# Performance work log

Measured on AMD Instinct MI355X. Metric: run time of the kernel, lower is better.

The kernel has to match this reference:

```python
import jax, jax.numpy as jnp
import numpy as np

B, C_IN, C_OUT, MODES, LENGTH = 32, 32, 32, 64, 16384


def dht(x):
    # Discrete Hartley Transform via complex FFT: H = Re(X) - Im(X) = sum x * cas
    X = jnp.fft.fft(x, axis=-1)
    return X.real - X.imag


def flip_periodic(x):
    # Z[0] = x[0], Z[k] = x[N-k] for k >= 1
    return jnp.concatenate([x[..., :1], x[..., 1:][..., ::-1]], axis=-1)


def setup_inputs() -> dict:
    key = jax.random.key(0)
    k1, k2, k3 = jax.random.split(key, 3)
    x = jax.random.normal(k1, (B, C_IN, LENGTH), dtype=jnp.float32)
    scale = 1.0 / (C_IN * C_OUT)
    weights1 = scale * jax.random.uniform(k2, (C_IN, C_OUT, MODES), dtype=jnp.float32)
    phase_weights = jax.random.uniform(k3, (C_IN, C_OUT, MODES), dtype=jnp.float32)
    return {"x": x, "weights1": weights1, "phase_weights": phase_weights}


def reference(x, weights1, phase_weights):
    batch, length = x.shape[0], x.shape[-1]
    m = weights1.shape[-1]
    out_ch = weights1.shape[1]

    x_ht = dht(x)                      # [b, in, L]
    xm = x_ht[:, :, :m]                # truncated spectrum [b, in, m]

    # Hartley convolution theorem: even/odd decomposition of the kernel
    y_flip = flip_periodic(weights1)
    y_even = 0.5 * (weights1 + y_flip)
    y_odd = 0.5 * (weights1 - y_flip)
    z = (jnp.einsum('bix,iox->box', xm, y_even)
         + jnp.einsum('bix,iox->box', flip_periodic(xm), y_odd))  # [b, out, m]

    # phase multiply (per-(out, mode); see notes on original in-place broadcast)
    z = z * jnp.sin(phase_weights)[0]  # [out, m] broadcast over batch

    out_ht = jnp.zeros((batch, out_ch, length), dtype=x.dtype).at[:, :, :m].set(z)
    # inverse DHT: DHT is involutory up to 1/n
    return dht(out_ht) / length
```

## Files before the change

kernel.cpp:

```cpp
#include <hip/hip_runtime.h>
#include <math.h>

#define N_LEN 16384
#define NMODES 64
#define NROWS 1024
#define TWO_PI_OVER_N 3.8349519697141029e-04f
#define PAD 72

typedef __bf16  bf16x8  __attribute__((ext_vector_type(8)));
typedef float   floatx16 __attribute__((ext_vector_type(16)));

__device__ inline unsigned short f2b(float f) {
    unsigned u = __float_as_uint(f);
    u += 0x7fffu + ((u >> 16) & 1u);
    return (unsigned short)(u >> 16);
}

__global__ __launch_bounds__(256) void build_tabs(unsigned short* __restrict__ Ttb,
                                                  unsigned short* __restrict__ Ttn) {
    int idx = blockIdx.x * 256 + threadIdx.x;
    int m, n;
    if (idx < N_LEN * NMODES) { m = idx >> 14; n = idx & (N_LEN - 1); }
    else { int j = idx - N_LEN * NMODES; n = j >> 6; m = j & 63; }
    float s, c;
    sincosf((float)((n * m) & (N_LEN - 1)) * TWO_PI_OVER_N, &s, &c);
    unsigned short v = f2b(c + s);
    if (idx < N_LEN * NMODES) Ttb[idx] = v;
    else                      Ttn[idx - N_LEN * NMODES] = v;
}

#define G1_RB 128

__global__ __launch_bounds__(256) void gemm1(const float* __restrict__ x,
                                             const unsigned short* __restrict__ Ttb,
                                             float* __restrict__ part,
                                             int ntiles) {
    __shared__ unsigned short xs[G1_RB * PAD];
    __shared__ unsigned short ts[64 * PAD];
    const int tid  = threadIdx.x;
    const int lane = tid & 63;
    const int w    = tid >> 6;
    const int q    = lane >> 5;
    const int m    = lane & 31;
    const int row0 = blockIdx.x * G1_RB;
    const int n0   = blockIdx.y * (ntiles * 64);

    floatx16 acc0, acc1;
#pragma unroll
    for (int i = 0; i < 16; ++i) { acc0[i] = 0.f; acc1[i] = 0.f; }

    float4 xr[8];
    uint4  tr[2];
    {
        const int base = n0;
#pragma unroll
        for (int it = 0; it < 8; ++it) {
            int cid = it * 256 + tid, rr = cid >> 4, cc = (cid & 15) * 4;
            xr[it] = *(const float4*)(x + (size_t)(row0 + rr) * N_LEN + base + cc);
        }
#pragma unroll
        for (int it = 0; it < 2; ++it) {
            int idx = it * 256 + tid, mm = idx >> 3, c = idx & 7;
            tr[it] = *(const uint4*)(Ttb + (size_t)mm * N_LEN + base + c * 8);
        }
    }

    for (int t = 0; t < ntiles; ++t) {
        __syncthreads();
#pragma unroll
        for (int it = 0; it < 8; ++it) {
            int cid = it * 256 + tid, rr = cid >> 4, cc = (cid & 15) * 4;
            ushort4 v;
            v.x = f2b(xr[it].x); v.y = f2b(xr[it].y);
            v.z = f2b(xr[it].z); v.w = f2b(xr[it].w);
            *(ushort4*)(xs + rr * PAD + cc) = v;
        }
#pragma unroll
        for (int it = 0; it < 2; ++it) {
            int idx = it * 256 + tid, mm = idx >> 3, c = idx & 7;
            *(uint4*)(ts + mm * PAD + c * 8) = tr[it];
        }
        if (t + 1 < ntiles) {
            const int base = n0 + (t + 1) * 64;
#pragma unroll
            for (int it = 0; it < 8; ++it) {
                int cid = it * 256 + tid, rr = cid >> 4, cc = (cid & 15) * 4;
                xr[it] = *(const float4*)(x + (size_t)(row0 + rr) * N_LEN + base + cc);
            }
#pragma unroll
            for (int it = 0; it < 2; ++it) {
                int idx = it * 256 + tid, mm = idx >> 3, c = idx & 7;
                tr[it] = *(const uint4*)(Ttb + (size_t)mm * N_LEN + base + c * 8);
            }
        }
        __syncthreads();
#pragma unroll
        for (int ks = 0; ks < 4; ++ks) {
            bf16x8 a  = *(const bf16x8*)(xs + (w * 32 + m) * PAD + ks * 16 + q * 8);
            bf16x8 b0 = *(const bf16x8*)(ts + (m)          * PAD + ks * 16 + q * 8);
            bf16x8 b1 = *(const bf16x8*)(ts + (32 + m)     * PAD + ks * 16 + q * 8);
            acc0 = __builtin_amdgcn_mfma_f32_32x32x16_bf16(a, b0, acc0, 0, 0, 0);
            acc1 = __builtin_amdgcn_mfma_f32_32x32x16_bf16(a, b1, acc1, 0, 0, 0);
        }
    }

    float* pb = part + ((size_t)blockIdx.y * NROWS + row0 + w * 32) * NMODES;
#pragma unroll
    for (int r = 0; r < 16; ++r) {
        int rowt = (r & 3) + 8 * (r >> 2) + 4 * q;
        pb[rowt * NMODES + m]      = acc0[r];
        pb[rowt * NMODES + 32 + m] = acc1[r];
    }
}

__global__ __launch_bounds__(256) void reduce_xm(const float* __restrict__ part,
                                                 float* __restrict__ xm, int S) {
    int gid = blockIdx.x * 256 + threadIdx.x;
    float4 a = make_float4(0.f, 0.f, 0.f, 0.f);
#pragma unroll 4
    for (int s = 0; s < S; ++s) {
        float4 v = *(const float4*)(part + (size_t)s * (NROWS * NMODES) + (size_t)gid * 4);
        a.x += v.x; a.y += v.y; a.z += v.z; a.w += v.w;
    }
    *(float4*)(xm + (size_t)gid * 4) = a;
}

__global__ __launch_bounds__(256) void mixk(const float* __restrict__ xm,
                                            const float* __restrict__ w1,
                                            const float* __restrict__ pw,
                                            unsigned short* __restrict__ zb) {
    int k = threadIdx.x & 63;
    int wave = threadIdx.x >> 6;
    int b = blockIdx.x;
    int o = blockIdx.y * 4 + wave;
    int kf = (NMODES - k) & 63;

    float acc = 0.f;
#pragma unroll 4
    for (int i = 0; i < 32; ++i) {
        float xv  = xm[(size_t)(b * 32 + i) * NMODES + k];
        float xvf = xm[(size_t)(b * 32 + i) * NMODES + kf];
        float w   = w1[(size_t)(i * 32 + o) * NMODES + k];
        float wf  = w1[(size_t)(i * 32 + o) * NMODES + kf];
        acc = fmaf(xv, 0.5f * (w + wf), acc);
        acc = fmaf(xvf, 0.5f * (w - wf), acc);
    }
    const float sc = 1.0f / (float)N_LEN;
    zb[(size_t)(b * 32 + o) * NMODES + k] =
        f2b(acc * sinf(pw[(size_t)o * NMODES + k]) * sc);
}

#define G2_NB 256

__global__ __launch_bounds__(256) void gemm2(const unsigned short* __restrict__ Ttn,
                                             const unsigned short* __restrict__ zb,
                                             float* __restrict__ out) {
    __shared__ unsigned short tts[G2_NB * PAD];
    __shared__ unsigned short zs[64 * PAD];
    const int tid  = threadIdx.x;
    const int lane = tid & 63;
    const int w    = tid >> 6;
    const int q    = lane >> 5;
    const int m    = lane & 31;
    const int wr   = w & 1;
    const int wn   = w >> 1;
    const int row0 = blockIdx.x * 64;
    const int nb0  = blockIdx.y * G2_NB;

#pragma unroll
    for (int it = 0; it < 8; ++it) {
        int idx = it * 256 + tid, rr = idx >> 3, c = idx & 7;
        *(uint4*)(tts + rr * PAD + c * 8) =
            *(const uint4*)(Ttn + (size_t)(nb0 + rr) * NMODES + c * 8);
    }
#pragma unroll
    for (int it = 0; it < 2; ++it) {
        int idx = it * 256 + tid, rr = idx >> 3, c = idx & 7;
        *(uint4*)(zs + rr * PAD + c * 8) =
            *(const uint4*)(zb + (size_t)(row0 + rr) * NMODES + c * 8);
    }
    __syncthreads();

    floatx16 acc[4];
#pragma unroll
    for (int nt = 0; nt < 4; ++nt)
#pragma unroll
        for (int i = 0; i < 16; ++i) acc[nt][i] = 0.f;

#pragma unroll
    for (int ks = 0; ks < 4; ++ks) {
        bf16x8 a = *(const bf16x8*)(zs + (wr * 32 + m) * PAD + ks * 16 + q * 8);
#pragma unroll
        for (int nt = 0; nt < 4; ++nt) {
            bf16x8 b = *(const bf16x8*)(tts + (wn * 128 + nt * 32 + m) * PAD + ks * 16 + q * 8);
            acc[nt] = __builtin_amdgcn_mfma_f32_32x32x16_bf16(a, b, acc[nt], 0, 0, 0);
        }
    }

#pragma unroll
    for (int nt = 0; nt < 4; ++nt) {
#pragma unroll
        for (int r = 0; r < 16; ++r) {
            int rowt = (r & 3) + 8 * (r >> 2) + 4 * q;
            out[(size_t)(row0 + wr * 32 + rowt) * N_LEN + nb0 + wn * 128 + nt * 32 + m]
                = acc[nt][r];
        }
    }
}

extern "C" void kernel_launch(void* const* d_in, const int* in_sizes, int n_in,
                              void* d_out, int out_size, void* d_ws, size_t ws_size,
                              hipStream_t stream) {
    const float* x  = (const float*)d_in[0];
    const float* w1 = (const float*)d_in[1];
    const float* pw = (const float*)d_in[2];
    float* out = (float*)d_out;

    int S = 64;
    while (S > 8) {
        size_t need = 2u * (size_t)N_LEN * NMODES * 2u
                    + (size_t)S * NROWS * NMODES * 4u
                    + (size_t)NROWS * NMODES * 4u
                    + (size_t)NROWS * NMODES * 2u;
        if (need <= ws_size) break;
        S >>= 1;
    }
    const int ntiles = N_LEN / S / 64;

    char* p = (char*)d_ws;
    unsigned short* Ttb = (unsigned short*)p;           p += (size_t)N_LEN * NMODES * 2;
    unsigned short* Ttn = (unsigned short*)p;           p += (size_t)N_LEN * NMODES * 2;
    float*          P   = (float*)p;                    p += (size_t)S * NROWS * NMODES * 4;
    float*          XM  = (float*)p;                    p += (size_t)NROWS * NMODES * 4;
    unsigned short* ZB  = (unsigned short*)p;

    build_tabs<<<dim3((2 * N_LEN * NMODES) / 256), dim3(256), 0, stream>>>(Ttb, Ttn);

    gemm1<<<dim3(NROWS / G1_RB, S), dim3(256), 0, stream>>>(x, Ttb, P, ntiles);

    reduce_xm<<<dim3(64), dim3(256), 0, stream>>>(P, XM, S);

    mixk<<<dim3(32, 8), dim3(256), 0, stream>>>(XM, w1, pw, ZB);

    gemm2<<<dim3(NROWS / 64, N_LEN / G2_NB), dim3(256), 0, stream>>>(Ttn, ZB, out);
}
```

Before: 146.4 us.

## Compute cas twiddles inline in both GEMMs instead of building global tables

Removes the build_tabs kernel and the two global bf16 cas tables. gemm1 and gemm2 now compute the cas values on the fly using hardware sin/cos in revolutions and write them straight into shared memory. This drops one launch and the table traffic through global memory, at the cost of redundant transcendental work in every block. reduce_xm is also reshaped to use scalar loads over four times as many threads with four independent accumulators, for more parallelism.

```diff
diff --git a/kernel.cpp b/kernel.cpp
--- a/kernel.cpp
+++ b/kernel.cpp
@@ -4,8 +4,8 @@
 #define N_LEN 16384
 #define NMODES 64
 #define NROWS 1024
-#define TWO_PI_OVER_N 3.8349519697141029e-04f
 #define PAD 72
+#define REV_SCALE 6.103515625e-05f
 
 typedef __bf16  bf16x8  __attribute__((ext_vector_type(8)));
 typedef float   floatx16 __attribute__((ext_vector_type(16)));
@@ -16,23 +16,21 @@
     return (unsigned short)(u >> 16);
 }
 
-__global__ __launch_bounds__(256) void build_tabs(unsigned short* __restrict__ Ttb,
-                                                  unsigned short* __restrict__ Ttn) {
-    int idx = blockIdx.x * 256 + threadIdx.x;
-    int m, n;
-    if (idx < N_LEN * NMODES) { m = idx >> 14; n = idx & (N_LEN - 1); }
-    else { int j = idx - N_LEN * NMODES; n = j >> 6; m = j & 63; }
+__device__ inline unsigned short cas_bf16(unsigned k) {
+    float rev = (float)k * REV_SCALE;
+#if __has_builtin(__builtin_amdgcn_sinf) && __has_builtin(__builtin_amdgcn_cosf)
+    float s = __builtin_amdgcn_sinf(rev);
+    float c = __builtin_amdgcn_cosf(rev);
+#else
     float s, c;
-    sincosf((float)((n * m) & (N_LEN - 1)) * TWO_PI_OVER_N, &s, &c);
-    unsigned short v = f2b(c + s);
-    if (idx < N_LEN * NMODES) Ttb[idx] = v;
-    else                      Ttn[idx - N_LEN * NMODES] = v;
+    sincosf(rev * 6.28318530717958647692f, &s, &c);
+#endif
+    return f2b(c + s);
 }
 
 #define G1_RB 128
 
 __global__ __launch_bounds__(256) void gemm1(const float* __restrict__ x,
-                                             const unsigned short* __restrict__ Ttb,
                                              float* __restrict__ part,
                                              int ntiles) {
     __shared__ unsigned short xs[G1_RB * PAD];
@@ -45,23 +43,20 @@
     const int row0 = blockIdx.x * G1_RB;
     const int n0   = blockIdx.y * (ntiles * 64);
 
+    const int mrow = tid >> 2;
+    const int nl0  = (tid & 3) * 16;
+
     floatx16 acc0, acc1;
 #pragma unroll
     for (int i = 0; i < 16; ++i) { acc0[i] = 0.f; acc1[i] = 0.f; }
 
     float4 xr[8];
-    uint4  tr[2];
     {
         const int base = n0;
 #pragma unroll
         for (int it = 0; it < 8; ++it) {
             int cid = it * 256 + tid, rr = cid >> 4, cc = (cid & 15) * 4;
             xr[it] = *(const float4*)(x + (size_t)(row0 + rr) * N_LEN + base + cc);
-        }
-#pragma unroll
-        for (int it = 0; it < 2; ++it) {
-            int idx = it * 256 + tid, mm = idx >> 3, c = idx & 7;
-            tr[it] = *(const uint4*)(Ttb + (size_t)mm * N_LEN + base + c * 8);
         }
     }
 
@@ -75,11 +70,6 @@
             v.z = f2b(xr[it].z); v.w = f2b(xr[it].w);
             *(ushort4*)(xs + rr * PAD + cc) = v;
         }
-#pragma unroll
-        for (int it = 0; it < 2; ++it) {
-            int idx = it * 256 + tid, mm = idx >> 3, c = idx & 7;
-            *(uint4*)(ts + mm * PAD + c * 8) = tr[it];
-        }
         if (t + 1 < ntiles) {
             const int base = n0 + (t + 1) * 64;
 #pragma unroll
@@ -87,11 +77,20 @@
                 int cid = it * 256 + tid, rr = cid >> 4, cc = (cid & 15) * 4;
                 xr[it] = *(const float4*)(x + (size_t)(row0 + rr) * N_LEN + base + cc);
             }
-#pragma unroll
-            for (int it = 0; it < 2; ++it) {
-                int idx = it * 256 + tid, mm = idx >> 3, c = idx & 7;
-                tr[it] = *(const uint4*)(Ttb + (size_t)mm * N_LEN + base + c * 8);
+        }
+        {
+            unsigned nb = (unsigned)(n0 + t * 64 + nl0);
+            unsigned k  = ((unsigned)mrow * nb) & (N_LEN - 1);
+            unsigned pk[8];
+#pragma unroll
+            for (int j = 0; j < 8; ++j) {
+                unsigned lo = cas_bf16(k); k = (k + mrow) & (N_LEN - 1);
+                unsigned hi = cas_bf16(k); k = (k + mrow) & (N_LEN - 1);
+                pk[j] = lo | (hi << 16);
             }
+            uint4* dst = (uint4*)(ts + mrow * PAD + nl0);
+            dst[0] = make_uint4(pk[0], pk[1], pk[2], pk[3]);
+            dst[1] = make_uint4(pk[4], pk[5], pk[6], pk[7]);
         }
         __syncthreads();
 #pragma unroll
@@ -116,13 +115,16 @@
 __global__ __launch_bounds__(256) void reduce_xm(const float* __restrict__ part,
                                                  float* __restrict__ xm, int S) {
     int gid = blockIdx.x * 256 + threadIdx.x;
-    float4 a = make_float4(0.f, 0.f, 0.f, 0.f);
+    const float* p = part + gid;
+    float a0 = 0.f, a1 = 0.f, a2 = 0.f, a3 = 0.f;
 #pragma unroll 4
-    for (int s = 0; s < S; ++s) {
-        float4 v = *(const float4*)(part + (size_t)s * (NROWS * NMODES) + (size_t)gid * 4);
-        a.x += v.x; a.y += v.y; a.z += v.z; a.w += v.w;
-    }
-    *(float4*)(xm + (size_t)gid * 4) = a;
+    for (int s = 0; s < S; s += 4) {
+        a0 += p[(size_t)(s + 0) * (NROWS * NMODES)];
+        a1 += p[(size_t)(s + 1) * (NROWS * NMODES)];
+        a2 += p[(size_t)(s + 2) * (NROWS * NMODES)];
+        a3 += p[(size_t)(s + 3) * (NROWS * NMODES)];
+    }
+    xm[gid] = (a0 + a1) + (a2 + a3);
 }
 
 __global__ __launch_bounds__(256) void mixk(const float* __restrict__ xm,
@@ -152,8 +154,7 @@
 
 #define G2_NB 256
 
-__global__ __launch_bounds__(256) void gemm2(const unsigned short* __restrict__ Ttn,
-                                             const unsigned short* __restrict__ zb,
+__global__ __launch_bounds__(256) void gemm2(const unsigned short* __restrict__ zb,
                                              float* __restrict__ out) {
     __shared__ unsigned short tts[G2_NB * PAD];
     __shared__ unsigned short zs[64 * PAD];
@@ -167,17 +168,34 @@
     const int row0 = blockIdx.x * 64;
     const int nb0  = blockIdx.y * G2_NB;
 
-#pragma unroll
-    for (int it = 0; it < 8; ++it) {
-        int idx = it * 256 + tid, rr = idx >> 3, c = idx & 7;
-        *(uint4*)(tts + rr * PAD + c * 8) =
-            *(const uint4*)(Ttn + (size_t)(nb0 + rr) * NMODES + c * 8);
-    }
+    uint4 zr[2];
 #pragma unroll
     for (int it = 0; it < 2; ++it) {
         int idx = it * 256 + tid, rr = idx >> 3, c = idx & 7;
-        *(uint4*)(zs + rr * PAD + c * 8) =
-            *(const uint4*)(zb + (size_t)(row0 + rr) * NMODES + c * 8);
+        zr[it] = *(const uint4*)(zb + (size_t)(row0 + rr) * NMODES + c * 8);
+    }
+
+    {
+        unsigned n = (unsigned)(nb0 + tid);
+        unsigned k = 0;
+        uint4* dst = (uint4*)(tts + tid * PAD);
+#pragma unroll
+        for (int g = 0; g < 8; ++g) {
+            unsigned pk[4];
+#pragma unroll
+            for (int j = 0; j < 4; ++j) {
+                unsigned lo = cas_bf16(k); k = (k + n) & (N_LEN - 1);
+                unsigned hi = cas_bf16(k); k = (k + n) & (N_LEN - 1);
+                pk[j] = lo | (hi << 16);
+            }
+            dst[g] = make_uint4(pk[0], pk[1], pk[2], pk[3]);
+        }
+    }
+
+#pragma unroll
+    for (int it = 0; it < 2; ++it) {
+        int idx = it * 256 + tid, rr = idx >> 3, c = idx & 7;
+        *(uint4*)(zs + rr * PAD + c * 8) = zr[it];
     }
     __syncthreads();
 
@@ -218,8 +236,7 @@
 
     int S = 64;
     while (S > 8) {
-        size_t need = 2u * (size_t)N_LEN * NMODES * 2u
-                    + (size_t)S * NROWS * NMODES * 4u
+        size_t need = (size_t)S * NROWS * NMODES * 4u
                     + (size_t)NROWS * NMODES * 4u
                     + (size_t)NROWS * NMODES * 2u;
         if (need <= ws_size) break;
@@ -228,19 +245,15 @@
     const int ntiles = N_LEN / S / 64;
 
     char* p = (char*)d_ws;
-    unsigned short* Ttb = (unsigned short*)p;           p += (size_t)N_LEN * NMODES * 2;
-    unsigned short* Ttn = (unsigned short*)p;           p += (size_t)N_LEN * NMODES * 2;
     float*          P   = (float*)p;                    p += (size_t)S * NROWS * NMODES * 4;
     float*          XM  = (float*)p;                    p += (size_t)NROWS * NMODES * 4;
     unsigned short* ZB  = (unsigned short*)p;
 
-    build_tabs<<<dim3((2 * N_LEN * NMODES) / 256), dim3(256), 0, stream>>>(Ttb, Ttn);
-
-    gemm1<<<dim3(NROWS / G1_RB, S), dim3(256), 0, stream>>>(x, Ttb, P, ntiles);
-
-    reduce_xm<<<dim3(64), dim3(256), 0, stream>>>(P, XM, S);
+    gemm1<<<dim3(NROWS / G1_RB, S), dim3(256), 0, stream>>>(x, P, ntiles);
+
+    reduce_xm<<<dim3(NROWS * NMODES / 256), dim3(256), 0, stream>>>(P, XM, S);
 
     mixk<<<dim3(32, 8), dim3(256), 0, stream>>>(XM, w1, pw, ZB);
 
-    gemm2<<<dim3(NROWS / 64, N_LEN / G2_NB), dim3(256), 0, stream>>>(Ttn, ZB, out);
-}
+    gemm2<<<dim3(NROWS / 64, N_LEN / G2_NB), dim3(256), 0, stream>>>(ZB, out);
+}
```

Result: faster. 134.1 us (-8.4%).
